# Kernel optimization log

Measured on AMD Instinct MI355X. Metric: run time of the kernel, lower is better.

The kernel has to match this reference:

```python
import jax, jax.numpy as jnp
import numpy as np
import math

PHI = (1.0 + math.sqrt(5.0)) / 2.0
EPS = 1e-10
QUBITS = 3
QDIM = 8  # 2 ** QUBITS
DIM = 4096
BATCH = 16384


def _pauli_sum(pauli, coeffs):
    """sum_i coeffs[i] * (I x ... x pauli_i x ... x I), shape [QDIM, QDIM]."""
    I2 = jnp.eye(2, dtype=jnp.complex64)
    total = jnp.zeros((QDIM, QDIM), jnp.complex64)
    for i in range(QUBITS):
        op = jnp.array([[1.0]], dtype=jnp.complex64)
        for j in range(QUBITS):
            op = jnp.kron(op, pauli if j == i else I2)
        total = total + coeffs[i].astype(jnp.complex64) * op
    return total


def _normalize(a):
    """QState constructor: a / ||a||, with fallback to |0> when norm < EPS."""
    norm = jnp.linalg.norm(a, axis=-1, keepdims=True)  # real [B,1]
    small = norm < EPS
    e0 = jnp.zeros_like(a).at[..., 0].set(1.0 + 0.0j)
    denom = jnp.where(small, 1.0, norm).astype(a.dtype)
    return jnp.where(small, e0, a / denom)


def setup_inputs() -> dict:
    key = jax.random.key(0)
    ks = jax.random.split(key, 6)
    bound_e = 1.0 / math.sqrt(DIM)
    bound_d = 1.0 / math.sqrt(QDIM)
    return {
        "x": jax.random.normal(ks[0], (BATCH, DIM), dtype=jnp.float32),
        "W_enc": jax.random.uniform(ks[1], (2 * QDIM, DIM), jnp.float32, -bound_e, bound_e),
        "b_enc": jax.random.uniform(ks[2], (2 * QDIM,), jnp.float32, -bound_e, bound_e),
        "phase": jnp.zeros((QDIM,), jnp.float32),
        "W_dec": jax.random.uniform(ks[3], (DIM, QDIM), jnp.float32, -bound_d, bound_d),
        "b_dec": jax.random.uniform(ks[4], (DIM,), jnp.float32, -bound_d, bound_d),
        "disorder": jax.random.normal(ks[5], (QUBITS,), jnp.float32) * 0.1,
    }


def reference(x, W_enc, b_enc, phase, W_dec, b_dec, disorder):
    B = x.shape[0]
    X = jnp.array([[0.0, 1.0], [1.0, 0.0]], dtype=jnp.complex64)
    Z = jnp.array([[1.0, 0.0], [0.0, -1.0]], dtype=jnp.complex64)
    Hx = _pauli_sum(X, jnp.ones((QUBITS,), jnp.float32))  # drive part (coeff applied later)
    Hz = _pauli_sum(Z, disorder)                           # disorder part

    # encode -> complex amplitudes with learned phase and bias
    enc = jnp.tanh(x @ W_enc.T + b_enc)               # [B, 2*QDIM]
    real, imag = enc[:, :QDIM], enc[:, QDIM:]
    amps = (real + 1j * imag) * jnp.exp(1j * phase * 0.1)[None, :]
    amps = amps + (0.05 / math.sqrt(QDIM))            # complex bias
    amps = _normalize(amps)                           # [B, QDIM] complex64

    # two first-order evolution steps; buffer t increments 0.02 per sample
    t0 = 0.02 * jnp.arange(B, dtype=jnp.float32)
    for step in range(2):
        t = t0 + 0.01 * step
        drive = (0.5 + 0.2 * jnp.sin(PHI * t)).astype(jnp.complex64)  # [B]
        # H(t) = drive*Hx + Hz is real symmetric, so H @ a == a @ H
        Ha = drive[:, None] * (amps @ Hx) + amps @ Hz
        amps = _normalize(amps - 1j * (0.01 * 0.01) * Ha)

    out = jnp.abs(amps) @ W_dec.T + b_dec             # [B, DIM]

    # final-state metrics (purity, coherence, entropy), averaged over batch
    rho = amps[:, :, None] * jnp.conj(amps)[:, None, :]           # [B,Q,Q]
    tr = jnp.real(jnp.einsum('bii->b', rho))
    rho = rho / (tr + EPS)[:, None, None]
    purity = jnp.real(jnp.einsum('bij,bji->b', rho, rho))
    off = jnp.where(jnp.eye(QDIM, dtype=bool)[None], 0.0, rho)
    coherence = jnp.sqrt(jnp.sum(jnp.abs(off) ** 2, axis=(1, 2)))
    ev = jnp.clip(jnp.linalg.eigvalsh(rho), EPS, 1.0)             # rho Hermitian -> real eigvals
    ev = ev / (jnp.sum(ev, axis=-1, keepdims=True) + EPS)
    entropy = -jnp.sum(ev * jnp.log2(ev + EPS), axis=-1)
    metrics = jnp.stack([purity.mean(), coherence.mean(), entropy.mean()])
    return out, metrics
```

## Files before the change

kernel.cpp:

```cpp
#include <hip/hip_runtime.h>

#define B_TOT 16384
#define DIMN  4096
#define EPSF  1e-10f

typedef __attribute__((ext_vector_type(8))) short bf16x8;
typedef __attribute__((ext_vector_type(4))) float f32x4;
typedef unsigned short u16;

__device__ __forceinline__ u16 f2bf(float f) {
  unsigned int u = __float_as_uint(f);
  u += 0x7FFFu + ((u >> 16) & 1u);
  return (u16)(u >> 16);
}
__device__ __forceinline__ unsigned int pk2(float a, float b) {
  return (unsigned int)f2bf(a) | ((unsigned int)f2bf(b) << 16);
}

__device__ __forceinline__ void normalize8(float* rr, float* ii) {
  float n2 = 0.f;
#pragma unroll
  for (int q = 0; q < 8; q++) n2 += rr[q] * rr[q] + ii[q] * ii[q];
  float n = sqrtf(n2);
  if (n < EPSF) {
#pragma unroll
    for (int q = 0; q < 8; q++) { rr[q] = 0.f; ii[q] = 0.f; }
    rr[0] = 1.f;
  } else {
    float inv = 1.f / n;
#pragma unroll
    for (int q = 0; q < 8; q++) { rr[q] *= inv; ii[q] *= inv; }
  }
}

__global__ __launch_bounds__(256) void k_prep(const float* __restrict__ wenc,
                                              u16* __restrict__ wbf) {
  int i = (blockIdx.x * 256 + threadIdx.x) * 4;
  float4 v = *reinterpret_cast<const float4*>(wenc + i);
  ushort4 o;
  o.x = f2bf(v.x); o.y = f2bf(v.y); o.z = f2bf(v.z); o.w = f2bf(v.w);
  *reinterpret_cast<ushort4*>(wbf + i) = o;
}

#define LDX(p)  (*reinterpret_cast<const float4*>(p))
#define LDW(p)  (*reinterpret_cast<const uint4*>(p))
#define MF(A0v, A1v, Bv)                                                    \
  do {                                                                      \
    union { unsigned int u[4]; bf16x8 v; } A_, B_;                          \
    A_.u[0] = pk2((A0v).x, (A0v).y); A_.u[1] = pk2((A0v).z, (A0v).w);       \
    A_.u[2] = pk2((A1v).x, (A1v).y); A_.u[3] = pk2((A1v).z, (A1v).w);       \
    B_.u[0] = (Bv).x; B_.u[1] = (Bv).y; B_.u[2] = (Bv).z; B_.u[3] = (Bv).w; \
    acc = __builtin_amdgcn_mfma_f32_16x16x32_bf16(A_.v, B_.v, acc, 0, 0, 0);\
  } while (0)

__global__ __launch_bounds__(256, 2) void k_encdec(
    const float* __restrict__ x, const u16* __restrict__ wbf,
    const float* __restrict__ benc, const float* __restrict__ phase,
    const float* __restrict__ disorder, const float* __restrict__ wdec,
    const float* __restrict__ bdec, float* __restrict__ out,
    float* __restrict__ blocksum) {
  __shared__ float encP[4 * 16 * 17];
  __shared__ float encL[16 * 17];
  __shared__ float absL[16 * 8];

  const int t = threadIdx.x;
  const int l = t & 63;
  const int h = t >> 6;
  const int r0 = blockIdx.x * 16;
  const int rloc = l & 15;
  const int koff = (l >> 4) * 8;

  const float* __restrict__ xp = x + (size_t)(r0 + rloc) * DIMN + h * 1024 + koff;
  const u16* __restrict__ wp = wbf + (size_t)rloc * DIMN + h * 1024 + koff;

  f32x4 acc = {0.f, 0.f, 0.f, 0.f};
  float4 a00 = LDX(xp +  0), a01 = LDX(xp +  4);
  float4 a10 = LDX(xp + 32), a11 = LDX(xp + 36);
  float4 a20 = LDX(xp + 64), a21 = LDX(xp + 68);
  float4 a30 = LDX(xp + 96), a31 = LDX(xp + 100);
  uint4 b0 = LDW(wp + 0), b1 = LDW(wp + 32), b2 = LDW(wp + 64), b3 = LDW(wp + 96);

  for (int g = 0; g < 7; ++g) {
    const int nb = (g * 4 + 4) * 32;
    MF(a00, a01, b0);
    a00 = LDX(xp + nb);      a01 = LDX(xp + nb + 4);      b0 = LDW(wp + nb);
    MF(a10, a11, b1);
    a10 = LDX(xp + nb + 32); a11 = LDX(xp + nb + 36);     b1 = LDW(wp + nb + 32);
    MF(a20, a21, b2);
    a20 = LDX(xp + nb + 64); a21 = LDX(xp + nb + 68);     b2 = LDW(wp + nb + 64);
    MF(a30, a31, b3);
    a30 = LDX(xp + nb + 96); a31 = LDX(xp + nb + 100);    b3 = LDW(wp + nb + 96);
  }
  MF(a00, a01, b0); MF(a10, a11, b1); MF(a20, a21, b2); MF(a30, a31, b3);

#pragma unroll
  for (int j = 0; j < 4; ++j)
    encP[h * 272 + ((l >> 4) * 4 + j) * 17 + rloc] = acc[j];
  __syncthreads();

  if (t < 64) {
#pragma unroll
    for (int p = 0; p < 4; ++p) {
      const int idx = t * 4 + p;
      const int row = idx >> 4, ft = idx & 15;
      encL[row * 17 + ft] = (encP[row * 17 + ft] + encP[272 + row * 17 + ft]) +
                            (encP[544 + row * 17 + ft] + encP[816 + row * 17 + ft]);
    }
  }
  __syncthreads();

  if (t < 16) {
    const int r = r0 + t;
    float e[16];
#pragma unroll
    for (int k = 0; k < 16; k++) e[k] = tanhf(encL[t * 17 + k] + benc[k]);

    float re[8], im[8];
#pragma unroll
    for (int q = 0; q < 8; q++) {
      float ph = 0.1f * phase[q];
      float cc = cosf(ph), ss = sinf(ph);
      re[q] = e[q] * cc - e[8 + q] * ss + 0.017677669529663688f;
      im[q] = e[q] * ss + e[8 + q] * cc;
    }
    normalize8(re, im);

    float dd0 = disorder[0], dd1 = disorder[1], dd2 = disorder[2];
    float hz[8];
#pragma unroll
    for (int i = 0; i < 8; i++)
      hz[i] = ((i & 4) ? -dd0 : dd0) + ((i & 2) ? -dd1 : dd1) + ((i & 1) ? -dd2 : dd2);

#pragma unroll
    for (int step = 0; step < 2; step++) {
      float tt = 0.02f * (float)r + 0.01f * (float)step;
      float drive = 0.5f + 0.2f * sinf(1.61803398874989485f * tt);
      float nr[8], ni[8];
#pragma unroll
      for (int j = 0; j < 8; j++) {
        float hr = drive * (re[j ^ 1] + re[j ^ 2] + re[j ^ 4]) + hz[j] * re[j];
        float hi = drive * (im[j ^ 1] + im[j ^ 2] + im[j ^ 4]) + hz[j] * im[j];
        nr[j] = re[j] + 1e-4f * hi;
        ni[j] = im[j] - 1e-4f * hr;
      }
      normalize8(nr, ni);
#pragma unroll
      for (int j = 0; j < 8; j++) { re[j] = nr[j]; im[j] = ni[j]; }
    }

    float tr = 0.f, s2 = 0.f;
#pragma unroll
    for (int q = 0; q < 8; q++) {
      float a2 = re[q] * re[q] + im[q] * im[q];
      tr += a2; s2 += a2 * a2;
      absL[t * 8 + q] = sqrtf(a2);
    }
    float trp = tr + EPSF;
    float purity = tr * tr / (trp * trp);
    float coh = sqrtf(fmaxf(tr * tr - s2, 0.f)) / trp;
    float lam = fminf(fmaxf(tr / trp, EPSF), 1.f);
    float denom = lam + 8.f * EPSF;
    float e1 = lam / denom, er = EPSF / denom;
    float ent = -(e1 * log2f(e1 + EPSF) + 7.f * er * log2f(er + EPSF));

    float sp = purity, sc2 = coh, sh = ent;
#pragma unroll
    for (int off = 8; off > 0; off >>= 1) {
      sp += __shfl_xor(sp, off);
      sc2 += __shfl_xor(sc2, off);
      sh += __shfl_xor(sh, off);
    }
    if (t == 0) {
      blocksum[blockIdx.x * 3 + 0] = sp;
      blocksum[blockIdx.x * 3 + 1] = sc2;
      blocksum[blockIdx.x * 3 + 2] = sh;
    }
  }
  __syncthreads();

#pragma unroll 1
  for (int g2 = 0; g2 < 4; ++g2) {
    const int c4 = g2 * 1024 + t * 4;
    float wd[4][8];
#pragma unroll
    for (int j = 0; j < 4; ++j) {
      float4 a = *reinterpret_cast<const float4*>(wdec + (size_t)(c4 + j) * 8);
      float4 b = *reinterpret_cast<const float4*>(wdec + (size_t)(c4 + j) * 8 + 4);
      wd[j][0] = a.x; wd[j][1] = a.y; wd[j][2] = a.z; wd[j][3] = a.w;
      wd[j][4] = b.x; wd[j][5] = b.y; wd[j][6] = b.z; wd[j][7] = b.w;
    }
    float4 bd = *reinterpret_cast<const float4*>(bdec + c4);
#pragma unroll
    for (int r = 0; r < 16; ++r) {
      float4 a0v = *reinterpret_cast<const float4*>(&absL[r * 8]);
      float4 a1v = *reinterpret_cast<const float4*>(&absL[r * 8 + 4]);
      float aq[8] = {a0v.x, a0v.y, a0v.z, a0v.w, a1v.x, a1v.y, a1v.z, a1v.w};
      float o0 = bd.x, o1 = bd.y, o2 = bd.z, o3 = bd.w;
#pragma unroll
      for (int q = 0; q < 8; ++q) {
        o0 = fmaf(aq[q], wd[0][q], o0);
        o1 = fmaf(aq[q], wd[1][q], o1);
        o2 = fmaf(aq[q], wd[2][q], o2);
        o3 = fmaf(aq[q], wd[3][q], o3);
      }
      *reinterpret_cast<float4*>(out + (size_t)(r0 + r) * DIMN + c4) =
          make_float4(o0, o1, o2, o3);
    }
  }
}

__global__ void k_final(const float* __restrict__ blocksum,
                        float* __restrict__ out) {
  const int t = threadIdx.x;
  float s0 = 0.f, s1 = 0.f, s2 = 0.f;
  for (int b = t; b < 1024; b += 64) {
    s0 += blocksum[b * 3 + 0];
    s1 += blocksum[b * 3 + 1];
    s2 += blocksum[b * 3 + 2];
  }
#pragma unroll
  for (int off = 32; off > 0; off >>= 1) {
    s0 += __shfl_down(s0, off);
    s1 += __shfl_down(s1, off);
    s2 += __shfl_down(s2, off);
  }
  if (t == 0) {
    out[(size_t)B_TOT * DIMN + 0] = s0 / 16384.f;
    out[(size_t)B_TOT * DIMN + 1] = s1 / 16384.f;
    out[(size_t)B_TOT * DIMN + 2] = s2 / 16384.f;
  }
}

extern "C" void kernel_launch(void* const* d_in, const int* in_sizes, int n_in,
                              void* d_out, int out_size, void* d_ws, size_t ws_size,
                              hipStream_t stream) {
  const float *x = nullptr, *wenc = nullptr, *benc = nullptr, *phase = nullptr,
              *wdec = nullptr, *bdec = nullptr, *dis = nullptr;
  for (int i = 0; i < n_in; i++) {
    switch (in_sizes[i]) {
      case 67108864: x = (const float*)d_in[i]; break;
      case 65536:    wenc = (const float*)d_in[i]; break;
      case 16:       benc = (const float*)d_in[i]; break;
      case 8:        phase = (const float*)d_in[i]; break;
      case 32768:    wdec = (const float*)d_in[i]; break;
      case 4096:     bdec = (const float*)d_in[i]; break;
      case 3:        dis = (const float*)d_in[i]; break;
      default: break;
    }
  }

  u16* wbf = (u16*)d_ws;
  float* bsum = (float*)d_ws + 32768;
  float* out = (float*)d_out;

  hipLaunchKernelGGL(k_prep, dim3(64), dim3(256), 0, stream, wenc, wbf);
  hipLaunchKernelGGL(k_encdec, dim3(1024), dim3(256), 0, stream,
                     x, wbf, benc, phase, dis, wdec, bdec, out, bsum);
  hipLaunchKernelGGL(k_final, dim3(1), dim3(64), 0, stream, bsum, out);
}
```

Before: 170.7 us.

## Warp-specialize encoder and decoder to overlap x reads with output writes

Each block now handles 32 rows in two 16-row tiles. Two waves run the MFMA encoder on the next tile while the other two waves run the decoder and write the output for the previous tile, using a double-buffered amplitude array. The goal is to overlap the 256 MB input read with the 256 MB output write instead of running them in sequence within each block. In exchange, half as many blocks launch, each phase uses only half the waves, the decoder work is split across three sync phases, and the encoder reduction per tile now comes from two waves instead of four.

```diff
diff --git a/kernel.cpp b/kernel.cpp
--- a/kernel.cpp
+++ b/kernel.cpp
@@ -53,159 +53,188 @@
     acc = __builtin_amdgcn_mfma_f32_16x16x32_bf16(A_.v, B_.v, acc, 0, 0, 0);\
   } while (0)
 
+__device__ __forceinline__ void dec_passes(const float* __restrict__ wdec,
+                                           const float* __restrict__ bdec,
+                                           float* __restrict__ out,
+                                           const float* __restrict__ absRow,
+                                           int rr, int t2, int p0, int p1) {
+  for (int p = p0; p < p1; ++p) {
+    const int c4 = p * 512 + t2 * 4;
+    float wd[4][8];
+#pragma unroll
+    for (int j = 0; j < 4; ++j) {
+      float4 a = *reinterpret_cast<const float4*>(wdec + (size_t)(c4 + j) * 8);
+      float4 b = *reinterpret_cast<const float4*>(wdec + (size_t)(c4 + j) * 8 + 4);
+      wd[j][0] = a.x; wd[j][1] = a.y; wd[j][2] = a.z; wd[j][3] = a.w;
+      wd[j][4] = b.x; wd[j][5] = b.y; wd[j][6] = b.z; wd[j][7] = b.w;
+    }
+    float4 bd = *reinterpret_cast<const float4*>(bdec + c4);
+#pragma unroll
+    for (int r = 0; r < 16; ++r) {
+      float4 a0v = *reinterpret_cast<const float4*>(&absRow[r * 8]);
+      float4 a1v = *reinterpret_cast<const float4*>(&absRow[r * 8 + 4]);
+      float aq[8] = {a0v.x, a0v.y, a0v.z, a0v.w, a1v.x, a1v.y, a1v.z, a1v.w};
+      float o0 = bd.x, o1 = bd.y, o2 = bd.z, o3 = bd.w;
+#pragma unroll
+      for (int q = 0; q < 8; ++q) {
+        o0 = fmaf(aq[q], wd[0][q], o0);
+        o1 = fmaf(aq[q], wd[1][q], o1);
+        o2 = fmaf(aq[q], wd[2][q], o2);
+        o3 = fmaf(aq[q], wd[3][q], o3);
+      }
+      *reinterpret_cast<float4*>(out + (size_t)(rr + r) * DIMN + c4) =
+          make_float4(o0, o1, o2, o3);
+    }
+  }
+}
+
 __global__ __launch_bounds__(256, 2) void k_encdec(
     const float* __restrict__ x, const u16* __restrict__ wbf,
     const float* __restrict__ benc, const float* __restrict__ phase,
     const float* __restrict__ disorder, const float* __restrict__ wdec,
     const float* __restrict__ bdec, float* __restrict__ out,
     float* __restrict__ blocksum) {
-  __shared__ float encP[4 * 16 * 17];
+  __shared__ float encP[2 * 16 * 17];
   __shared__ float encL[16 * 17];
-  __shared__ float absL[16 * 8];
+  __shared__ float absL[2][128];
 
   const int t = threadIdx.x;
+  const int r0 = blockIdx.x * 32;
+  float ms0 = 0.f, ms1 = 0.f, ms2 = 0.f;
+
   const int l = t & 63;
-  const int h = t >> 6;
-  const int r0 = blockIdx.x * 16;
+  const int w01 = (t >> 6) & 1;
   const int rloc = l & 15;
   const int koff = (l >> 4) * 8;
-
-  const float* __restrict__ xp = x + (size_t)(r0 + rloc) * DIMN + h * 1024 + koff;
-  const u16* __restrict__ wp = wbf + (size_t)rloc * DIMN + h * 1024 + koff;
-
-  f32x4 acc = {0.f, 0.f, 0.f, 0.f};
-  float4 a00 = LDX(xp +  0), a01 = LDX(xp +  4);
-  float4 a10 = LDX(xp + 32), a11 = LDX(xp + 36);
-  float4 a20 = LDX(xp + 64), a21 = LDX(xp + 68);
-  float4 a30 = LDX(xp + 96), a31 = LDX(xp + 100);
-  uint4 b0 = LDW(wp + 0), b1 = LDW(wp + 32), b2 = LDW(wp + 64), b3 = LDW(wp + 96);
-
-  for (int g = 0; g < 7; ++g) {
-    const int nb = (g * 4 + 4) * 32;
-    MF(a00, a01, b0);
-    a00 = LDX(xp + nb);      a01 = LDX(xp + nb + 4);      b0 = LDW(wp + nb);
-    MF(a10, a11, b1);
-    a10 = LDX(xp + nb + 32); a11 = LDX(xp + nb + 36);     b1 = LDW(wp + nb + 32);
-    MF(a20, a21, b2);
-    a20 = LDX(xp + nb + 64); a21 = LDX(xp + nb + 68);     b2 = LDW(wp + nb + 64);
-    MF(a30, a31, b3);
-    a30 = LDX(xp + nb + 96); a31 = LDX(xp + nb + 100);    b3 = LDW(wp + nb + 96);
-  }
-  MF(a00, a01, b0); MF(a10, a11, b1); MF(a20, a21, b2); MF(a30, a31, b3);
-
-#pragma unroll
-  for (int j = 0; j < 4; ++j)
-    encP[h * 272 + ((l >> 4) * 4 + j) * 17 + rloc] = acc[j];
-  __syncthreads();
-
-  if (t < 64) {
-#pragma unroll
-    for (int p = 0; p < 4; ++p) {
-      const int idx = t * 4 + p;
-      const int row = idx >> 4, ft = idx & 15;
-      encL[row * 17 + ft] = (encP[row * 17 + ft] + encP[272 + row * 17 + ft]) +
-                            (encP[544 + row * 17 + ft] + encP[816 + row * 17 + ft]);
-    }
-  }
-  __syncthreads();
-
-  if (t < 16) {
-    const int r = r0 + t;
-    float e[16];
-#pragma unroll
-    for (int k = 0; k < 16; k++) e[k] = tanhf(encL[t * 17 + k] + benc[k]);
-
-    float re[8], im[8];
-#pragma unroll
-    for (int q = 0; q < 8; q++) {
-      float ph = 0.1f * phase[q];
-      float cc = cosf(ph), ss = sinf(ph);
-      re[q] = e[q] * cc - e[8 + q] * ss + 0.017677669529663688f;
-      im[q] = e[q] * ss + e[8 + q] * cc;
-    }
-    normalize8(re, im);
-
-    float dd0 = disorder[0], dd1 = disorder[1], dd2 = disorder[2];
-    float hz[8];
-#pragma unroll
-    for (int i = 0; i < 8; i++)
-      hz[i] = ((i & 4) ? -dd0 : dd0) + ((i & 2) ? -dd1 : dd1) + ((i & 1) ? -dd2 : dd2);
-
-#pragma unroll
-    for (int step = 0; step < 2; step++) {
-      float tt = 0.02f * (float)r + 0.01f * (float)step;
-      float drive = 0.5f + 0.2f * sinf(1.61803398874989485f * tt);
-      float nr[8], ni[8];
-#pragma unroll
-      for (int j = 0; j < 8; j++) {
-        float hr = drive * (re[j ^ 1] + re[j ^ 2] + re[j ^ 4]) + hz[j] * re[j];
-        float hi = drive * (im[j ^ 1] + im[j ^ 2] + im[j ^ 4]) + hz[j] * im[j];
-        nr[j] = re[j] + 1e-4f * hi;
-        ni[j] = im[j] - 1e-4f * hr;
-      }
-      normalize8(nr, ni);
-#pragma unroll
-      for (int j = 0; j < 8; j++) { re[j] = nr[j]; im[j] = ni[j]; }
-    }
-
-    float tr = 0.f, s2 = 0.f;
-#pragma unroll
-    for (int q = 0; q < 8; q++) {
-      float a2 = re[q] * re[q] + im[q] * im[q];
-      tr += a2; s2 += a2 * a2;
-      absL[t * 8 + q] = sqrtf(a2);
-    }
-    float trp = tr + EPSF;
-    float purity = tr * tr / (trp * trp);
-    float coh = sqrtf(fmaxf(tr * tr - s2, 0.f)) / trp;
-    float lam = fminf(fmaxf(tr / trp, EPSF), 1.f);
-    float denom = lam + 8.f * EPSF;
-    float e1 = lam / denom, er = EPSF / denom;
-    float ent = -(e1 * log2f(e1 + EPSF) + 7.f * er * log2f(er + EPSF));
-
-    float sp = purity, sc2 = coh, sh = ent;
-#pragma unroll
-    for (int off = 8; off > 0; off >>= 1) {
-      sp += __shfl_xor(sp, off);
-      sc2 += __shfl_xor(sc2, off);
-      sh += __shfl_xor(sh, off);
-    }
-    if (t == 0) {
-      blocksum[blockIdx.x * 3 + 0] = sp;
-      blocksum[blockIdx.x * 3 + 1] = sc2;
-      blocksum[blockIdx.x * 3 + 2] = sh;
-    }
-  }
-  __syncthreads();
-
-#pragma unroll 1
-  for (int g2 = 0; g2 < 4; ++g2) {
-    const int c4 = g2 * 1024 + t * 4;
-    float wd[4][8];
-#pragma unroll
-    for (int j = 0; j < 4; ++j) {
-      float4 a = *reinterpret_cast<const float4*>(wdec + (size_t)(c4 + j) * 8);
-      float4 b = *reinterpret_cast<const float4*>(wdec + (size_t)(c4 + j) * 8 + 4);
-      wd[j][0] = a.x; wd[j][1] = a.y; wd[j][2] = a.z; wd[j][3] = a.w;
-      wd[j][4] = b.x; wd[j][5] = b.y; wd[j][6] = b.z; wd[j][7] = b.w;
-    }
-    float4 bd = *reinterpret_cast<const float4*>(bdec + c4);
-#pragma unroll
-    for (int r = 0; r < 16; ++r) {
-      float4 a0v = *reinterpret_cast<const float4*>(&absL[r * 8]);
-      float4 a1v = *reinterpret_cast<const float4*>(&absL[r * 8 + 4]);
-      float aq[8] = {a0v.x, a0v.y, a0v.z, a0v.w, a1v.x, a1v.y, a1v.z, a1v.w};
-      float o0 = bd.x, o1 = bd.y, o2 = bd.z, o3 = bd.w;
-#pragma unroll
-      for (int q = 0; q < 8; ++q) {
-        o0 = fmaf(aq[q], wd[0][q], o0);
-        o1 = fmaf(aq[q], wd[1][q], o1);
-        o2 = fmaf(aq[q], wd[2][q], o2);
-        o3 = fmaf(aq[q], wd[3][q], o3);
-      }
-      *reinterpret_cast<float4*>(out + (size_t)(r0 + r) * DIMN + c4) =
-          make_float4(o0, o1, o2, o3);
-    }
+  const int t2 = t & 127;
+
+  for (int it = 0; it < 3; ++it) {
+    const int pt = it, ct = it - 1;
+
+    if (t < 128) {
+      if (pt < 2) {
+        const float* __restrict__ xp =
+            x + (size_t)(r0 + pt * 16 + rloc) * DIMN + w01 * 2048 + koff;
+        const u16* __restrict__ wp =
+            wbf + (size_t)rloc * DIMN + w01 * 2048 + koff;
+        f32x4 acc = {0.f, 0.f, 0.f, 0.f};
+        float4 a00 = LDX(xp +  0), a01 = LDX(xp +  4);
+        float4 a10 = LDX(xp + 32), a11 = LDX(xp + 36);
+        float4 a20 = LDX(xp + 64), a21 = LDX(xp + 68);
+        float4 a30 = LDX(xp + 96), a31 = LDX(xp + 100);
+        uint4 b0 = LDW(wp + 0), b1 = LDW(wp + 32), b2 = LDW(wp + 64), b3 = LDW(wp + 96);
+        for (int g = 0; g < 15; ++g) {
+          const int nb = (g * 4 + 4) * 32;
+          MF(a00, a01, b0);
+          a00 = LDX(xp + nb);      a01 = LDX(xp + nb + 4);      b0 = LDW(wp + nb);
+          MF(a10, a11, b1);
+          a10 = LDX(xp + nb + 32); a11 = LDX(xp + nb + 36);     b1 = LDW(wp + nb + 32);
+          MF(a20, a21, b2);
+          a20 = LDX(xp + nb + 64); a21 = LDX(xp + nb + 68);     b2 = LDW(wp + nb + 64);
+          MF(a30, a31, b3);
+          a30 = LDX(xp + nb + 96); a31 = LDX(xp + nb + 100);    b3 = LDW(wp + nb + 96);
+        }
+        MF(a00, a01, b0); MF(a10, a11, b1); MF(a20, a21, b2); MF(a30, a31, b3);
+#pragma unroll
+        for (int j = 0; j < 4; ++j)
+          encP[w01 * 272 + ((l >> 4) * 4 + j) * 17 + rloc] = acc[j];
+      }
+    } else {
+      if (ct >= 0)
+        dec_passes(wdec, bdec, out, absL[ct & 1], r0 + ct * 16, t2, 0, 4);
+    }
+    __syncthreads();
+
+    if (t < 128) {
+      if (pt < 2 && t < 64) {
+#pragma unroll
+        for (int p = 0; p < 4; ++p) {
+          const int idx = t * 4 + p;
+          const int row = idx >> 4, ft = idx & 15;
+          encL[row * 17 + ft] = encP[row * 17 + ft] + encP[272 + row * 17 + ft];
+        }
+      }
+    } else {
+      if (ct >= 0)
+        dec_passes(wdec, bdec, out, absL[ct & 1], r0 + ct * 16, t2, 4, 6);
+    }
+    __syncthreads();
+
+    if (t < 128) {
+      if (pt < 2 && t < 16) {
+        const int r = r0 + pt * 16 + t;
+        float e[16];
+#pragma unroll
+        for (int k = 0; k < 16; k++) e[k] = tanhf(encL[t * 17 + k] + benc[k]);
+
+        float re[8], im[8];
+#pragma unroll
+        for (int q = 0; q < 8; q++) {
+          float ph = 0.1f * phase[q];
+          float cc = cosf(ph), ss = sinf(ph);
+          re[q] = e[q] * cc - e[8 + q] * ss + 0.017677669529663688f;
+          im[q] = e[q] * ss + e[8 + q] * cc;
+        }
+        normalize8(re, im);
+
+        float dd0 = disorder[0], dd1 = disorder[1], dd2 = disorder[2];
+        float hz[8];
+#pragma unroll
+        for (int i = 0; i < 8; i++)
+          hz[i] = ((i & 4) ? -dd0 : dd0) + ((i & 2) ? -dd1 : dd1) + ((i & 1) ? -dd2 : dd2);
+
+#pragma unroll
+        for (int step = 0; step < 2; step++) {
+          float tt = 0.02f * (float)r + 0.01f * (float)step;
+          float drive = 0.5f + 0.2f * sinf(1.61803398874989485f * tt);
+          float nr[8], ni[8];
+#pragma unroll
+          for (int j = 0; j < 8; j++) {
+            float hr = drive * (re[j ^ 1] + re[j ^ 2] + re[j ^ 4]) + hz[j] * re[j];
+            float hi = drive * (im[j ^ 1] + im[j ^ 2] + im[j ^ 4]) + hz[j] * im[j];
+            nr[j] = re[j] + 1e-4f * hi;
+            ni[j] = im[j] - 1e-4f * hr;
+          }
+          normalize8(nr, ni);
+#pragma unroll
+          for (int j = 0; j < 8; j++) { re[j] = nr[j]; im[j] = ni[j]; }
+        }
+
+        float tr = 0.f, s2 = 0.f;
+#pragma unroll
+        for (int q = 0; q < 8; q++) {
+          float a2 = re[q] * re[q] + im[q] * im[q];
+          tr += a2; s2 += a2 * a2;
+          absL[pt & 1][t * 8 + q] = sqrtf(a2);
+        }
+        float trp = tr + EPSF;
+        float purity = tr * tr / (trp * trp);
+        float coh = sqrtf(fmaxf(tr * tr - s2, 0.f)) / trp;
+        float lam = fminf(fmaxf(tr / trp, EPSF), 1.f);
+        float denom = lam + 8.f * EPSF;
+        float e1 = lam / denom, er = EPSF / denom;
+        float ent = -(e1 * log2f(e1 + EPSF) + 7.f * er * log2f(er + EPSF));
+
+        float sp = purity, sc2 = coh, sh = ent;
+#pragma unroll
+        for (int off = 8; off > 0; off >>= 1) {
+          sp += __shfl_xor(sp, off);
+          sc2 += __shfl_xor(sc2, off);
+          sh += __shfl_xor(sh, off);
+        }
+        if (t == 0) { ms0 += sp; ms1 += sc2; ms2 += sh; }
+      }
+    } else {
+      if (ct >= 0)
+        dec_passes(wdec, bdec, out, absL[ct & 1], r0 + ct * 16, t2, 6, 8);
+    }
+    __syncthreads();
+  }
+
+  if (t == 0) {
+    blocksum[blockIdx.x * 3 + 0] = ms0;
+    blocksum[blockIdx.x * 3 + 1] = ms1;
+    blocksum[blockIdx.x * 3 + 2] = ms2;
   }
 }
 
@@ -213,7 +242,7 @@
                         float* __restrict__ out) {
   const int t = threadIdx.x;
   float s0 = 0.f, s1 = 0.f, s2 = 0.f;
-  for (int b = t; b < 1024; b += 64) {
+  for (int b = t; b < 512; b += 64) {
     s0 += blocksum[b * 3 + 0];
     s1 += blocksum[b * 3 + 1];
     s2 += blocksum[b * 3 + 2];
@@ -254,7 +283,7 @@
   float* out = (float*)d_out;
 
   hipLaunchKernelGGL(k_prep, dim3(64), dim3(256), 0, stream, wenc, wbf);
-  hipLaunchKernelGGL(k_encdec, dim3(1024), dim3(256), 0, stream,
+  hipLaunchKernelGGL(k_encdec, dim3(512), dim3(256), 0, stream,
                      x, wbf, benc, phase, dis, wdec, bdec, out, bsum);
   hipLaunchKernelGGL(k_final, dim3(1), dim3(64), 0, stream, bsum, out);
 }
```

Result: slower. 621.2 us (+264.0%).
